# Kernel optimization log

Hardware: AMD Instinct MI355X
Metric: run time of the kernel (lower is better)

Reference implementation:

```python
import jax, jax.numpy as jnp
import numpy as np

N_NODES = 50000
N_EDGES = 800000
D_IN = 96
D_OUT = 96


def setup_inputs() -> dict:
    key = jax.random.key(0)
    k1, k2, k3, k4, k5, k6 = jax.random.split(key, 6)
    x = jax.random.normal(k1, (N_NODES, D_IN), dtype=jnp.float32)
    edge_index = jax.random.randint(k2, (2, N_EDGES), 0, N_NODES, dtype=jnp.int32)
    W_lin = jax.random.normal(k3, (D_OUT, D_IN), dtype=jnp.float32) * 0.1
    b_lin = jax.random.normal(k4, (D_OUT,), dtype=jnp.float32) * 0.1
    W_root = jax.random.normal(k5, (D_OUT, D_IN), dtype=jnp.float32) * 0.1
    b_root = jax.random.normal(k6, (D_OUT,), dtype=jnp.float32) * 0.1
    return {"x": x, "edge_index": edge_index, "W_lin": W_lin, "b_lin": b_lin,
            "W_root": W_root, "b_root": b_root}


def reference(x, edge_index, W_lin, b_lin, W_root, b_root):
    # GCNConv with separate root weight: out = relu(scatter_add(norm * lin(x_src), dst) + root(x))
    src, dst = edge_index[0], edge_index[1]
    n = x.shape[0]
    # symmetric degree normalization (in-degree based, clamped to avoid div0)
    deg = jax.ops.segment_sum(jnp.ones(src.shape[0], dtype=x.dtype), dst, num_segments=n)
    dinv = jax.lax.rsqrt(jnp.maximum(deg, 1.0))
    norm = dinv[src] * dinv[dst]                      # [E]
    h = x @ W_lin.T + b_lin                           # [N, D_OUT] neighbor transform
    msgs = h[src] * norm[:, None]                     # [E, D_OUT] gathered + scaled
    agg = jax.ops.segment_sum(msgs, dst, num_segments=n)  # scatter-add
    out = agg + x @ W_root.T + b_root                 # root/self contribution
    return jax.nn.relu(out)
```

## Files before the change

kernel.cpp:

```cpp
#include <hip/hip_runtime.h>

#define D 96
#define BSH 5
#define SCAP 1088
#define SBSH 8
#define NSBMAX 224
#define SBCAP 4608
#define CH 2048

typedef __attribute__((ext_vector_type(8))) short bf16x8;
typedef __attribute__((ext_vector_type(4))) float f32x4;

__device__ __forceinline__ unsigned bf16_rne(float f) {
    unsigned u = __float_as_uint(f);
    return (u + 0x7fffu + ((u >> 16) & 1u)) >> 16;
}
__device__ __forceinline__ float blo(unsigned u) { return __uint_as_float(u << 16); }
__device__ __forceinline__ float bhi(unsigned u) { return __uint_as_float(u & 0xffff0000u); }

__global__ __launch_bounds__(512) void bin_kernel(
    const int* __restrict__ ei, int* __restrict__ scur, unsigned* __restrict__ sp,
    const float* __restrict__ Wlin, const float* __restrict__ Wroot,
    unsigned* __restrict__ wfrag, int E, int NSB)
{
    __shared__ int hist[NSBMAX];
    __shared__ int lstart[NSBMAX];
    __shared__ int gbase[NSBMAX];
    __shared__ unsigned stage[CH];
    int t = threadIdx.x;
    int gt = blockIdx.x * 512 + t;
    int e0 = blockIdx.x * CH;
    int ne = min(CH, E - e0);
    for (int i = t; i < NSB; i += 512) hist[i] = 0;
    if (gt < 9216) {
        int f = gt >> 8, r = gt & 255;
        int l = r >> 2, jp = r & 3;
        int ct = f / 6, st = f % 6;
        int nn = ct * 16 + (l & 15);
        int k  = st * 32 + (l >> 4) * 8 + jp * 2;
        const float* W = (k < D) ? Wlin : Wroot;
        int kk = (k < D) ? k : k - D;
        float v0 = W[nn * D + kk], v1 = W[nn * D + kk + 1];
        wfrag[gt] = bf16_rne(v0) | (bf16_rne(v1) << 16);
    }
    __syncthreads();
    unsigned pk[4]; int bk[4];
    int base = e0 + t * 4;
    if (base + 3 < E) {
        int4 a = *(const int4*)(ei + base);
        int4 b = *(const int4*)(ei + E + base);
        pk[0] = (unsigned)a.x | ((unsigned)b.x << 16); bk[0] = b.x >> SBSH;
        pk[1] = (unsigned)a.y | ((unsigned)b.y << 16); bk[1] = b.y >> SBSH;
        pk[2] = (unsigned)a.z | ((unsigned)b.z << 16); bk[2] = b.z >> SBSH;
        pk[3] = (unsigned)a.w | ((unsigned)b.w << 16); bk[3] = b.w >> SBSH;
    } else {
        #pragma unroll
        for (int u = 0; u < 4; ++u) {
            int e = base + u;
            if (e < E) { pk[u] = (unsigned)ei[e] | ((unsigned)ei[E + e] << 16); bk[u] = ei[E + e] >> SBSH; }
            else bk[u] = -1;
        }
    }
    #pragma unroll
    for (int u = 0; u < 4; ++u)
        if (bk[u] >= 0) atomicAdd(&hist[bk[u]], 1);
    __syncthreads();
    if (t < 64) {
        int carry = 0;
        for (int c0 = 0; c0 < NSB; c0 += 64) {
            int i = c0 + t;
            int v = (i < NSB) ? hist[i] : 0;
            int incl = v;
            #pragma unroll
            for (int d = 1; d < 64; d <<= 1) {
                int uu = __shfl_up(incl, d, 64);
                if (t >= d) incl += uu;
            }
            if (i < NSB) lstart[i] = carry + incl - v;
            carry += __shfl(incl, 63, 64);
        }
    }
    __syncthreads();
    for (int i = t; i < NSB; i += 512) {
        int c = hist[i];
        if (c > 0) gbase[i] = atomicAdd(&scur[i], c);
        hist[i] = lstart[i];
    }
    __syncthreads();
    #pragma unroll
    for (int u = 0; u < 4; ++u) {
        if (bk[u] >= 0) {
            int p = atomicAdd(&hist[bk[u]], 1);
            stage[p] = pk[u];
        }
    }
    __syncthreads();
    for (int i = t; i < ne; i += 512) {
        unsigned w = stage[i];
        int sb = (int)(w >> (16 + SBSH));
        int slot = gbase[sb] + (i - lstart[sb]);
        if (slot < SBCAP) sp[(size_t)sb * SBCAP + slot] = w;
    }
}

__global__ __launch_bounds__(256) void xspack_kernel(
    const float* __restrict__ x, unsigned* __restrict__ xs, int n)
{
    int gt = blockIdx.x * 256 + threadIdx.x;
    int gsz = gridDim.x * 256;
    int ntask = (n + 1) * 24;
    for (int i = gt; i < ntask; i += gsz) {
        int row = i / 24, q = i - row * 24;
        uint2 o;
        if (row < n) {
            float4 v = ((const float4*)x)[(size_t)row * 24 + q];
            o.x = bf16_rne(v.x) | (bf16_rne(v.y) << 16);
            o.y = bf16_rne(v.z) | (bf16_rne(v.w) << 16);
        } else { o.x = 0u; o.y = 0u; }
        *(uint2*)(xs + (size_t)row * 48 + q * 2) = o;
    }
}

__global__ __launch_bounds__(512) void dinv_kernel(
    const int* __restrict__ scur, const unsigned* __restrict__ sp,
    float* __restrict__ dinv, int n)
{
    __shared__ int hist[256];
    int t = threadIdx.x;
    if (t < 256) hist[t] = 0;
    __syncthreads();
    int ne = min(scur[blockIdx.x], SBCAP);
    const unsigned* spb = sp + (size_t)blockIdx.x * SBCAP;
    for (int i0 = t * 4; i0 < ne; i0 += 2048) {
        if (i0 + 3 < ne) {
            uint4 w = *(const uint4*)(spb + i0);
            atomicAdd(&hist[(w.x >> 16) & 255], 1);
            atomicAdd(&hist[(w.y >> 16) & 255], 1);
            atomicAdd(&hist[(w.z >> 16) & 255], 1);
            atomicAdd(&hist[(w.w >> 16) & 255], 1);
        } else {
            for (int i = i0; i < ne; ++i) atomicAdd(&hist[(spb[i] >> 16) & 255], 1);
        }
    }
    __syncthreads();
    if (t < 256) {
        int node = (blockIdx.x << SBSH) + t;
        if (node < n) {
            int d = hist[t];
            dinv[node] = rsqrtf((float)(d > 1 ? d : 1));
        }
    }
    if (blockIdx.x == 0 && t == 256) dinv[n] = 0.f;
}

__global__ __launch_bounds__(256, 8) void bgather_gemm_kernel(
    const int* __restrict__ scur, const unsigned* __restrict__ sp,
    const float* __restrict__ dinv, const unsigned* __restrict__ xs,
    const unsigned* __restrict__ wfrag, const float* __restrict__ blin,
    const float* __restrict__ broot, float* __restrict__ out, int n)
{
    __shared__ uint2 sd[SCAP];
    __shared__ int hist[32];
    __shared__ int seg[33];
    __shared__ int cur[32];
    __shared__ int pq;
    __shared__ unsigned yt[32][52];
    __shared__ float sv32[32];
    int t = threadIdx.x;
    int nwg = gridDim.x;
    int qq = nwg >> 3, rr = nwg & 7;
    int xcd = blockIdx.x & 7, ix = blockIdx.x >> 3;
    int bid = (xcd < rr ? xcd * (qq + 1) : rr * (qq + 1) + (xcd - rr) * qq) + ix;
    int node0 = bid << BSH;
    int sb = bid >> 3;
    int lb = bid & 7;
    int ne = min(scur[sb], SBCAP);
    const unsigned* spb = sp + (size_t)sb * SBCAP;
    const unsigned ZR = (unsigned)n;
    if (t < 32) hist[t] = 0;
    if (t < 8) sd[t] = make_uint2(ZR, 0u);
    __syncthreads();
    for (int i0 = t * 4; i0 < ne; i0 += 1024) {
        if (i0 + 3 < ne) {
            uint4 w4 = *(const uint4*)(spb + i0);
            if (((w4.x >> (16 + BSH)) & 7) == (unsigned)lb) atomicAdd(&hist[(w4.x >> 16) & 31], 1);
            if (((w4.y >> (16 + BSH)) & 7) == (unsigned)lb) atomicAdd(&hist[(w4.y >> 16) & 31], 1);
            if (((w4.z >> (16 + BSH)) & 7) == (unsigned)lb) atomicAdd(&hist[(w4.z >> 16) & 31], 1);
            if (((w4.w >> (16 + BSH)) & 7) == (unsigned)lb) atomicAdd(&hist[(w4.w >> 16) & 31], 1);
        } else {
            for (int i = i0; i < ne; ++i) {
                unsigned w = spb[i];
                if (((w >> (16 + BSH)) & 7) == (unsigned)lb) atomicAdd(&hist[(w >> 16) & 31], 1);
            }
        }
    }
    __syncthreads();
    if (t == 0) {
        int run = 8;
        #pragma unroll
        for (int i = 0; i < 32; ++i) {
            seg[i] = run;
            run += (hist[i] + 7) & ~7;
            if (run > SCAP) run = SCAP;
        }
        seg[32] = run;
        pq = 0;
    }
    __syncthreads();
    if (t < 32) cur[t] = seg[t];
    __syncthreads();
    for (int i0 = t * 4; i0 < ne; i0 += 1024) {
        if (i0 + 3 < ne) {
            uint4 w4 = *(const uint4*)(spb + i0);
            if (((w4.x >> (16 + BSH)) & 7) == (unsigned)lb) { int p = atomicAdd(&cur[(w4.x >> 16) & 31], 1); if (p < SCAP) sd[p].x = w4.x & 0xffffu; }
            if (((w4.y >> (16 + BSH)) & 7) == (unsigned)lb) { int p = atomicAdd(&cur[(w4.y >> 16) & 31], 1); if (p < SCAP) sd[p].x = w4.y & 0xffffu; }
            if (((w4.z >> (16 + BSH)) & 7) == (unsigned)lb) { int p = atomicAdd(&cur[(w4.z >> 16) & 31], 1); if (p < SCAP) sd[p].x = w4.z & 0xffffu; }
            if (((w4.w >> (16 + BSH)) & 7) == (unsigned)lb) { int p = atomicAdd(&cur[(w4.w >> 16) & 31], 1); if (p < SCAP) sd[p].x = w4.w & 0xffffu; }
        } else {
            for (int i = i0; i < ne; ++i) {
                unsigned w = spb[i];
                if (((w >> (16 + BSH)) & 7) == (unsigned)lb) { int p = atomicAdd(&cur[(w >> 16) & 31], 1); if (p < SCAP) sd[p].x = w & 0xffffu; }
            }
        }
    }
    __syncthreads();
    if (t < 32) {
        int e = seg[t + 1];
        int s = seg[t] + hist[t]; if (s > e) s = e;
        for (int p2 = s; p2 < e; ++p2) sd[p2] = make_uint2(ZR, 0u);
    }
    __syncthreads();
    int tot = seg[32];
    for (int i = t; i < tot; i += 256) sd[i].y = __float_as_uint(dinv[sd[i].x]);
    __syncthreads();

    int l = t & 63;
    int g = l / 12;
    int m = l - g * 12;
    unsigned loff = (unsigned)(m << 4);
    const char* xb = (const char*)xs;

    for (;;) {
        int p;
        if (l == 0) p = atomicAdd(&pq, 1);
        p = __builtin_amdgcn_readfirstlane(p);
        if (p >= 16) break;
        int ndA = p * 2, ndB = ndA + 1;
        int jsA = seg[ndA], itA = (seg[ndA + 1] - jsA) >> 3;
        int jsB = seg[ndB], itB = (seg[ndB + 1] - jsB) >> 3;
        int iters = itA > itB ? itA : itB;
        float aA0=0.f,aA1=0.f,aA2=0.f,aA3=0.f,aA4=0.f,aA5=0.f,aA6=0.f,aA7=0.f;
        float aB0=0.f,aB1=0.f,aB2=0.f,aB3=0.f,aB4=0.f,aB5=0.f,aB6=0.f,aB7=0.f;
        float sn = 0.f;
        for (int it = 0; it < iters; ++it) {
            int baseA = (it < itA) ? (jsA + it * 8) : 0;
            int baseB = (it < itB) ? (jsB + it * 8) : 0;
            if (l < 48) {
                uint2 qA0 = sd[baseA + g], qA1 = sd[baseA + 4 + g];
                uint2 qB0 = sd[baseB + g], qB1 = sd[baseB + 4 + g];
                uint4 vA0 = *(const uint4*)(xb + qA0.x * 192u + loff);
                uint4 vA1 = *(const uint4*)(xb + qA1.x * 192u + loff);
                uint4 vB0 = *(const uint4*)(xb + qB0.x * 192u + loff);
                uint4 vB1 = *(const uint4*)(xb + qB1.x * 192u + loff);
                float dA0 = __uint_as_float(qA0.y), dA1 = __uint_as_float(qA1.y);
                float dB0 = __uint_as_float(qB0.y), dB1 = __uint_as_float(qB1.y);
                aA0 += dA0 * blo(vA0.x); aA1 += dA0 * bhi(vA0.x); aA2 += dA0 * blo(vA0.y); aA3 += dA0 * bhi(vA0.y);
                aA4 += dA0 * blo(vA0.z); aA5 += dA0 * bhi(vA0.z); aA6 += dA0 * blo(vA0.w); aA7 += dA0 * bhi(vA0.w);
                aA0 += dA1 * blo(vA1.x); aA1 += dA1 * bhi(vA1.x); aA2 += dA1 * blo(vA1.y); aA3 += dA1 * bhi(vA1.y);
                aA4 += dA1 * blo(vA1.z); aA5 += dA1 * bhi(vA1.z); aA6 += dA1 * blo(vA1.w); aA7 += dA1 * bhi(vA1.w);
                aB0 += dB0 * blo(vB0.x); aB1 += dB0 * bhi(vB0.x); aB2 += dB0 * blo(vB0.y); aB3 += dB0 * bhi(vB0.y);
                aB4 += dB0 * blo(vB0.z); aB5 += dB0 * bhi(vB0.z); aB6 += dB0 * blo(vB0.w); aB7 += dB0 * bhi(vB0.w);
                aB0 += dB1 * blo(vB1.x); aB1 += dB1 * bhi(vB1.x); aB2 += dB1 * blo(vB1.y); aB3 += dB1 * bhi(vB1.y);
                aB4 += dB1 * blo(vB1.z); aB5 += dB1 * bhi(vB1.z); aB6 += dB1 * blo(vB1.w); aB7 += dB1 * bhi(vB1.w);
            } else {
                int bs = (l < 56) ? baseA : baseB;
                sn += __uint_as_float(sd[bs + (l & 7)].y);
            }
        }
        float stA = 0.f, stB = 0.f;
        #pragma unroll
        for (int u = 0; u < 8; ++u) {
            stA += __shfl(sn, 48 + u, 64);
            stB += __shfl(sn, 56 + u, 64);
        }
        int l24 = (l + 24) & 63, l12 = (l + 12) & 63;
        aA0 += __shfl(aA0, l24, 64); aA1 += __shfl(aA1, l24, 64); aA2 += __shfl(aA2, l24, 64); aA3 += __shfl(aA3, l24, 64);
        aA4 += __shfl(aA4, l24, 64); aA5 += __shfl(aA5, l24, 64); aA6 += __shfl(aA6, l24, 64); aA7 += __shfl(aA7, l24, 64);
        aB0 += __shfl(aB0, l24, 64); aB1 += __shfl(aB1, l24, 64); aB2 += __shfl(aB2, l24, 64); aB3 += __shfl(aB3, l24, 64);
        aB4 += __shfl(aB4, l24, 64); aB5 += __shfl(aB5, l24, 64); aB6 += __shfl(aB6, l24, 64); aB7 += __shfl(aB7, l24, 64);
        aA0 += __shfl(aA0, l12, 64); aA1 += __shfl(aA1, l12, 64); aA2 += __shfl(aA2, l12, 64); aA3 += __shfl(aA3, l12, 64);
        aA4 += __shfl(aA4, l12, 64); aA5 += __shfl(aA5, l12, 64); aA6 += __shfl(aA6, l12, 64); aA7 += __shfl(aA7, l12, 64);
        aB0 += __shfl(aB0, l12, 64); aB1 += __shfl(aB1, l12, 64); aB2 += __shfl(aB2, l12, 64); aB3 += __shfl(aB3, l12, 64);
        aB4 += __shfl(aB4, l12, 64); aB5 += __shfl(aB5, l12, 64); aB6 += __shfl(aB6, l12, 64); aB7 += __shfl(aB7, l12, 64);
        int nodeA = node0 + ndA, nodeB = node0 + ndB;
        float dnA = (nodeA < n) ? dinv[nodeA] : 0.f;
        float dnB = (nodeB < n) ? dinv[nodeB] : 0.f;
        if (l < 12) {
            uint4 oA, oB;
            oA.x = bf16_rne(dnA * aA0) | (bf16_rne(dnA * aA1) << 16);
            oA.y = bf16_rne(dnA * aA2) | (bf16_rne(dnA * aA3) << 16);
            oA.z = bf16_rne(dnA * aA4) | (bf16_rne(dnA * aA5) << 16);
            oA.w = bf16_rne(dnA * aA6) | (bf16_rne(dnA * aA7) << 16);
            oB.x = bf16_rne(dnB * aB0) | (bf16_rne(dnB * aB1) << 16);
            oB.y = bf16_rne(dnB * aB2) | (bf16_rne(dnB * aB3) << 16);
            oB.z = bf16_rne(dnB * aB4) | (bf16_rne(dnB * aB5) << 16);
            oB.w = bf16_rne(dnB * aB6) | (bf16_rne(dnB * aB7) << 16);
            *(uint4*)&yt[ndA][4 * m] = oA;
            *(uint4*)&yt[ndB][4 * m] = oB;
        } else if (l == 48) {
            sv32[ndA] = dnA * stA;
            sv32[ndB] = dnB * stB;
        }
    }
    __syncthreads();

    int wv = t >> 6;
    int lane15 = l & 15, quad = l >> 4;
    for (int j = wv; j < 12; j += 4) {
        int rg = j / 6, ct = j % 6;
        int r0 = node0 + rg * 16;
        f32x4 accY = (f32x4){0.f, 0.f, 0.f, 0.f};
        f32x4 accX = (f32x4){0.f, 0.f, 0.f, 0.f};
        #pragma unroll
        for (int st_ = 0; st_ < 3; ++st_) {
            bf16x8 a = *(const bf16x8*)(&yt[rg * 16 + lane15][st_ * 16 + quad * 4]);
            bf16x8 b = *(const bf16x8*)(wfrag + ((ct * 6 + st_) * 64 + l) * 4);
            accY = __builtin_amdgcn_mfma_f32_16x16x32_bf16(a, b, accY, 0, 0, 0);
        }
        int ar = r0 + lane15;
        #pragma unroll
        for (int sm = 0; sm < 3; ++sm) {
            bf16x8 a = (bf16x8){0, 0, 0, 0, 0, 0, 0, 0};
            if (ar < n) a = *(const bf16x8*)(xs + (size_t)ar * 48 + sm * 16 + quad * 4);
            bf16x8 b = *(const bf16x8*)(wfrag + ((ct * 6 + 3 + sm) * 64 + l) * 4);
            accX = __builtin_amdgcn_mfma_f32_16x16x32_bf16(a, b, accX, 0, 0, 0);
        }
        int col = ct * 16 + lane15;
        float blc = blin[col], brc = broot[col];
        #pragma unroll
        for (int reg = 0; reg < 4; ++reg) {
            int r = r0 + quad * 4 + reg;
            if (r < n) {
                float sv = sv32[rg * 16 + quad * 4 + reg];
                float v = accY[reg] + accX[reg] + sv * blc + brc;
                out[(size_t)r * D + col] = fmaxf(v, 0.f);
            }
        }
    }
}

extern "C" void kernel_launch(void* const* d_in, const int* in_sizes, int n_in,
                              void* d_out, int out_size, void* d_ws, size_t ws_size,
                              hipStream_t stream) {
    const float* x     = (const float*)d_in[0];
    const int*   ei    = (const int*)d_in[1];
    const float* Wlin  = (const float*)d_in[2];
    const float* blin  = (const float*)d_in[3];
    const float* Wroot = (const float*)d_in[4];
    const float* broot = (const float*)d_in[5];
    float* out = (float*)d_out;

    const int n = in_sizes[0] / D;
    const int E = in_sizes[1] / 2;
    const int NB = (n + 31) >> BSH;
    const int NSB = (n + 255) >> SBSH;

    int*      scur  = (int*)d_ws;
    float*    dinv  = (float*)(scur + 256);
    unsigned* sp    = (unsigned*)(dinv + n + 4);
    unsigned* wfrag = sp + (size_t)NSB * SBCAP;
    unsigned* xs    = wfrag + 9216;

    hipMemsetAsync(scur, 0, 256 * sizeof(int), stream);

    bin_kernel<<<(E + CH - 1) / CH, 512, 0, stream>>>(ei, scur, sp, Wlin, Wroot,
                                                      wfrag, E, NSB);
    xspack_kernel<<<1024, 256, 0, stream>>>(x, xs, n);
    dinv_kernel<<<NSB, 512, 0, stream>>>(scur, sp, dinv, n);
    bgather_gemm_kernel<<<NB, 256, 0, stream>>>(scur, sp, dinv, xs, wfrag,
                                                blin, broot, out, n);
}
```

Baseline: 141.2 us.

## Replace atomic bucket binning with deterministic histogram-scan-scatter passes

The single binning kernel, which claimed global slots through atomics on per-bucket counters, is split into three passes. A histogram kernel writes per-block bucket counts, a scan kernel computes per-bucket block offsets, and a scatter kernel places edges at those offsets. The x-to-bf16 packing is folded into the histogram kernel and the memset is dropped. This removes global atomics and gives deterministic edge ordering within each bucket, but adds a kernel launch and reads the edge index twice.

New measurement: 143.0 us. About the same (+1.3%).

```diff
diff --git a/kernel.cpp b/kernel.cpp
--- a/kernel.cpp
+++ b/kernel.cpp
@@ -18,19 +18,16 @@
 __device__ __forceinline__ float blo(unsigned u) { return __uint_as_float(u << 16); }
 __device__ __forceinline__ float bhi(unsigned u) { return __uint_as_float(u & 0xffff0000u); }
 
-__global__ __launch_bounds__(512) void bin_kernel(
-    const int* __restrict__ ei, int* __restrict__ scur, unsigned* __restrict__ sp,
+__global__ __launch_bounds__(512) void hist_kernel(
+    const int* __restrict__ ei, int* __restrict__ ghist,
     const float* __restrict__ Wlin, const float* __restrict__ Wroot,
-    unsigned* __restrict__ wfrag, int E, int NSB)
+    unsigned* __restrict__ wfrag, const float* __restrict__ x,
+    unsigned* __restrict__ xs, int E, int NSB, int NBLK, int n)
 {
     __shared__ int hist[NSBMAX];
-    __shared__ int lstart[NSBMAX];
-    __shared__ int gbase[NSBMAX];
-    __shared__ unsigned stage[CH];
     int t = threadIdx.x;
     int gt = blockIdx.x * 512 + t;
     int e0 = blockIdx.x * CH;
-    int ne = min(CH, E - e0);
     for (int i = t; i < NSB; i += 512) hist[i] = 0;
     if (gt < 9216) {
         int f = gt >> 8, r = gt & 255;
@@ -43,6 +40,70 @@
         float v0 = W[nn * D + kk], v1 = W[nn * D + kk + 1];
         wfrag[gt] = bf16_rne(v0) | (bf16_rne(v1) << 16);
     }
+    __syncthreads();
+    int base = e0 + t * 4;
+    if (base + 3 < E) {
+        int4 b = *(const int4*)(ei + E + base);
+        atomicAdd(&hist[b.x >> SBSH], 1);
+        atomicAdd(&hist[b.y >> SBSH], 1);
+        atomicAdd(&hist[b.z >> SBSH], 1);
+        atomicAdd(&hist[b.w >> SBSH], 1);
+    } else {
+        for (int u = 0; u < 4; ++u) {
+            int e = base + u;
+            if (e < E) atomicAdd(&hist[ei[E + e] >> SBSH], 1);
+        }
+    }
+    __syncthreads();
+    for (int i = t; i < NSB; i += 512) ghist[(size_t)i * NBLK + blockIdx.x] = hist[i];
+    int gsz = gridDim.x * 512;
+    int ntask = (n + 1) * 24;
+    for (int i = gt; i < ntask; i += gsz) {
+        int row = i / 24, q = i - row * 24;
+        uint2 o;
+        if (row < n) {
+            float4 v = ((const float4*)x)[(size_t)row * 24 + q];
+            o.x = bf16_rne(v.x) | (bf16_rne(v.y) << 16);
+            o.y = bf16_rne(v.z) | (bf16_rne(v.w) << 16);
+        } else { o.x = 0u; o.y = 0u; }
+        *(uint2*)(xs + (size_t)row * 48 + q * 2) = o;
+    }
+}
+
+__global__ __launch_bounds__(64) void scan_kernel(
+    int* __restrict__ ghist, int* __restrict__ scur, int NBLK)
+{
+    int t = threadIdx.x;
+    int* row = ghist + (size_t)blockIdx.x * NBLK;
+    int carry = 0;
+    for (int c0 = 0; c0 < NBLK; c0 += 64) {
+        int i = c0 + t;
+        int v = (i < NBLK) ? row[i] : 0;
+        int incl = v;
+        #pragma unroll
+        for (int d = 1; d < 64; d <<= 1) {
+            int uu = __shfl_up(incl, d, 64);
+            if (t >= d) incl += uu;
+        }
+        if (i < NBLK) row[i] = carry + incl - v;
+        carry += __shfl(incl, 63, 64);
+    }
+    if (t == 0) scur[blockIdx.x] = carry;
+}
+
+__global__ __launch_bounds__(512) void scatter_kernel(
+    const int* __restrict__ ei, const int* __restrict__ ghist,
+    unsigned* __restrict__ sp, int E, int NSB, int NBLK)
+{
+    __shared__ int hist[NSBMAX];
+    __shared__ int lstart[NSBMAX];
+    __shared__ int gb[NSBMAX];
+    __shared__ unsigned stage[CH];
+    int t = threadIdx.x;
+    int blk = blockIdx.x;
+    int e0 = blk * CH;
+    int ne = min(CH, E - e0);
+    for (int i = t; i < NSB; i += 512) hist[i] = 0;
     __syncthreads();
     unsigned pk[4]; int bk[4];
     int base = e0 + t * 4;
@@ -82,8 +143,7 @@
     }
     __syncthreads();
     for (int i = t; i < NSB; i += 512) {
-        int c = hist[i];
-        if (c > 0) gbase[i] = atomicAdd(&scur[i], c);
+        gb[i] = ghist[(size_t)i * NBLK + blk];
         hist[i] = lstart[i];
     }
     __syncthreads();
@@ -98,26 +158,8 @@
     for (int i = t; i < ne; i += 512) {
         unsigned w = stage[i];
         int sb = (int)(w >> (16 + SBSH));
-        int slot = gbase[sb] + (i - lstart[sb]);
+        int slot = gb[sb] + (i - lstart[sb]);
         if (slot < SBCAP) sp[(size_t)sb * SBCAP + slot] = w;
-    }
-}
-
-__global__ __launch_bounds__(256) void xspack_kernel(
-    const float* __restrict__ x, unsigned* __restrict__ xs, int n)
-{
-    int gt = blockIdx.x * 256 + threadIdx.x;
-    int gsz = gridDim.x * 256;
-    int ntask = (n + 1) * 24;
-    for (int i = gt; i < ntask; i += gsz) {
-        int row = i / 24, q = i - row * 24;
-        uint2 o;
-        if (row < n) {
-            float4 v = ((const float4*)x)[(size_t)row * 24 + q];
-            o.x = bf16_rne(v.x) | (bf16_rne(v.y) << 16);
-            o.y = bf16_rne(v.z) | (bf16_rne(v.w) << 16);
-        } else { o.x = 0u; o.y = 0u; }
-        *(uint2*)(xs + (size_t)row * 48 + q * 2) = o;
     }
 }
 
@@ -364,18 +406,19 @@
     const int E = in_sizes[1] / 2;
     const int NB = (n + 31) >> BSH;
     const int NSB = (n + 255) >> SBSH;
+    const int NBLK = (E + CH - 1) / CH;
 
     int*      scur  = (int*)d_ws;
     float*    dinv  = (float*)(scur + 256);
     unsigned* sp    = (unsigned*)(dinv + n + 4);
     unsigned* wfrag = sp + (size_t)NSB * SBCAP;
     unsigned* xs    = wfrag + 9216;
-
-    hipMemsetAsync(scur, 0, 256 * sizeof(int), stream);
-
-    bin_kernel<<<(E + CH - 1) / CH, 512, 0, stream>>>(ei, scur, sp, Wlin, Wroot,
-                                                      wfrag, E, NSB);
-    xspack_kernel<<<1024, 256, 0, stream>>>(x, xs, n);
+    int*      ghist = (int*)(xs + (size_t)(n + 1) * 48);
+
+    hist_kernel<<<NBLK, 512, 0, stream>>>(ei, ghist, Wlin, Wroot, wfrag,
+                                          x, xs, E, NSB, NBLK, n);
+    scan_kernel<<<NSB, 64, 0, stream>>>(ghist, scur, NBLK);
+    scatter_kernel<<<NBLK, 512, 0, stream>>>(ei, ghist, sp, E, NSB, NBLK);
     dinv_kernel<<<NSB, 512, 0, stream>>>(scur, sp, dinv, n);
     bgather_gemm_kernel<<<NB, 256, 0, stream>>>(scur, sp, dinv, xs, wfrag,
                                                 blin, broot, out, n);
```

## Fuse binning, packing, degree and gather-GEMM into one cooperative kernel

Applied to the files above, without the earlier changes.

Merges the four separate launches (edge binning, x bf16 packing, degree/dinv, gather+MFMA GEMM) into one persistent kernel with grid-wide syncs between phases. The aim is to remove launch gaps and kernel-boundary drains. Binning now runs at 256 threads with 8 edges per thread, and all phases share one raw shared-memory buffer. If cooperative launch fails, it falls back to three launches selected by mask. Risks: grid sync cost, NB=1563 blocks must all be co-resident (7 per CU), and occupancy drops from 8 to 7 blocks per CU.

Result: slower. 498.7 us (+253.3%).

```diff
diff --git a/kernel.cpp b/kernel.cpp
--- a/kernel.cpp
+++ b/kernel.cpp
@@ -1,4 +1,7 @@
 #include <hip/hip_runtime.h>
+#include <hip/hip_cooperative_groups.h>
+
+namespace cg = cooperative_groups;
 
 #define D 96
 #define BSH 5
@@ -7,6 +10,7 @@
 #define NSBMAX 224
 #define SBCAP 4608
 #define CH 2048
+#define SMBYTES 15888
 
 typedef __attribute__((ext_vector_type(8))) short bf16x8;
 typedef __attribute__((ext_vector_type(4))) float f32x4;
@@ -18,332 +22,322 @@
 __device__ __forceinline__ float blo(unsigned u) { return __uint_as_float(u << 16); }
 __device__ __forceinline__ float bhi(unsigned u) { return __uint_as_float(u & 0xffff0000u); }
 
-__global__ __launch_bounds__(512) void bin_kernel(
+__global__ __launch_bounds__(256, 7) void fused_kernel(
     const int* __restrict__ ei, int* __restrict__ scur, unsigned* __restrict__ sp,
     const float* __restrict__ Wlin, const float* __restrict__ Wroot,
-    unsigned* __restrict__ wfrag, int E, int NSB)
+    unsigned* __restrict__ wfrag, const float* __restrict__ x,
+    unsigned* __restrict__ xs, float* __restrict__ dinv, int* __restrict__ deg,
+    const float* __restrict__ blin, const float* __restrict__ broot,
+    float* __restrict__ out, int E, int NSB, int NBLK, int n, int mask)
 {
-    __shared__ int hist[NSBMAX];
-    __shared__ int lstart[NSBMAX];
-    __shared__ int gbase[NSBMAX];
-    __shared__ unsigned stage[CH];
+    __shared__ __attribute__((aligned(16))) char smraw[SMBYTES];
     int t = threadIdx.x;
-    int gt = blockIdx.x * 512 + t;
-    int e0 = blockIdx.x * CH;
-    int ne = min(CH, E - e0);
-    for (int i = t; i < NSB; i += 512) hist[i] = 0;
-    if (gt < 9216) {
-        int f = gt >> 8, r = gt & 255;
-        int l = r >> 2, jp = r & 3;
-        int ct = f / 6, st = f % 6;
-        int nn = ct * 16 + (l & 15);
-        int k  = st * 32 + (l >> 4) * 8 + jp * 2;
-        const float* W = (k < D) ? Wlin : Wroot;
-        int kk = (k < D) ? k : k - D;
-        float v0 = W[nn * D + kk], v1 = W[nn * D + kk + 1];
-        wfrag[gt] = bf16_rne(v0) | (bf16_rne(v1) << 16);
+    int blk = blockIdx.x;
+
+    if (mask & 1) {
+        int gt = blk * 256 + t;
+        if (gt < 9216) {
+            int f = gt >> 8, r = gt & 255;
+            int l = r >> 2, jp = r & 3;
+            int ct = f / 6, st = f % 6;
+            int nn = ct * 16 + (l & 15);
+            int k  = st * 32 + (l >> 4) * 8 + jp * 2;
+            const float* W = (k < D) ? Wlin : Wroot;
+            int kk = (k < D) ? k : k - D;
+            float v0 = W[nn * D + kk], v1 = W[nn * D + kk + 1];
+            wfrag[gt] = bf16_rne(v0) | (bf16_rne(v1) << 16);
+        }
+        if (blk < NBLK) {
+            int* histA   = (int*)smraw;
+            int* lstartA = histA + NSBMAX;
+            int* gbaseA  = lstartA + NSBMAX;
+            unsigned* stageA = (unsigned*)(gbaseA + NSBMAX);
+            int e0 = blk * CH;
+            int ne = min(CH, E - e0);
+            for (int i = t; i < NSB; i += 256) histA[i] = 0;
+            __syncthreads();
+            unsigned pk[8]; int bk[8];
+            int base = e0 + t * 8;
+            #pragma unroll
+            for (int q = 0; q < 2; ++q) {
+                int b4 = base + q * 4;
+                if (b4 + 3 < E) {
+                    int4 a = *(const int4*)(ei + b4);
+                    int4 b = *(const int4*)(ei + E + b4);
+                    pk[q*4+0] = (unsigned)a.x | ((unsigned)b.x << 16); bk[q*4+0] = b.x >> SBSH;
+                    pk[q*4+1] = (unsigned)a.y | ((unsigned)b.y << 16); bk[q*4+1] = b.y >> SBSH;
+                    pk[q*4+2] = (unsigned)a.z | ((unsigned)b.z << 16); bk[q*4+2] = b.z >> SBSH;
+                    pk[q*4+3] = (unsigned)a.w | ((unsigned)b.w << 16); bk[q*4+3] = b.w >> SBSH;
+                } else {
+                    #pragma unroll
+                    for (int u = 0; u < 4; ++u) {
+                        int e = b4 + u;
+                        if (e < E) { pk[q*4+u] = (unsigned)ei[e] | ((unsigned)ei[E + e] << 16); bk[q*4+u] = ei[E + e] >> SBSH; }
+                        else bk[q*4+u] = -1;
+                    }
+                }
+            }
+            #pragma unroll
+            for (int u = 0; u < 8; ++u)
+                if (bk[u] >= 0) atomicAdd(&histA[bk[u]], 1);
+            __syncthreads();
+            if (t < 64) {
+                int carry = 0;
+                for (int c0 = 0; c0 < NSB; c0 += 64) {
+                    int i = c0 + t;
+                    int v = (i < NSB) ? histA[i] : 0;
+                    int incl = v;
+                    #pragma unroll
+                    for (int d = 1; d < 64; d <<= 1) {
+                        int uu = __shfl_up(incl, d, 64);
+                        if (t >= d) incl += uu;
+                    }
+                    if (i < NSB) lstartA[i] = carry + incl - v;
+                    carry += __shfl(incl, 63, 64);
+                }
+            }
+            __syncthreads();
+            for (int i = t; i < NSB; i += 256) {
+                int c = histA[i];
+                if (c > 0) gbaseA[i] = atomicAdd(&scur[i], c);
+                histA[i] = lstartA[i];
+            }
+            __syncthreads();
+            #pragma unroll
+            for (int u = 0; u < 8; ++u) {
+                if (bk[u] >= 0) {
+                    int p = atomicAdd(&histA[bk[u]], 1);
+                    stageA[p] = pk[u];
+                }
+            }
+            __syncthreads();
+            for (int i = t; i < ne; i += 256) {
+                unsigned w = stageA[i];
+                int sb = (int)(w >> (16 + SBSH));
+                int slot = gbaseA[sb] + (i - lstartA[sb]);
+                if (slot < SBCAP) sp[(size_t)sb * SBCAP + slot] = w;
+            }
+        }
+        int gsz = gridDim.x * 256;
+        int ntask = (n + 1) * 24;
+        for (int i = blk * 256 + t; i < ntask; i += gsz) {
+            int row = i / 24, q = i - row * 24;
+            uint2 o;
+            if (row < n) {
+                float4 v = ((const float4*)x)[(size_t)row * 24 + q];
+                o.x = bf16_rne(v.x) | (bf16_rne(v.y) << 16);
+                o.y = bf16_rne(v.z) | (bf16_rne(v.w) << 16);
+            } else { o.x = 0u; o.y = 0u; }
+            *(uint2*)(xs + (size_t)row * 48 + q * 2) = o;
+        }
     }
-    __syncthreads();
-    unsigned pk[4]; int bk[4];
-    int base = e0 + t * 4;
-    if (base + 3 < E) {
-        int4 a = *(const int4*)(ei + base);
-        int4 b = *(const int4*)(ei + E + base);
-        pk[0] = (unsigned)a.x | ((unsigned)b.x << 16); bk[0] = b.x >> SBSH;
-        pk[1] = (unsigned)a.y | ((unsigned)b.y << 16); bk[1] = b.y >> SBSH;
-        pk[2] = (unsigned)a.z | ((unsigned)b.z << 16); bk[2] = b.z >> SBSH;
-        pk[3] = (unsigned)a.w | ((unsigned)b.w << 16); bk[3] = b.w >> SBSH;
-    } else {
-        #pragma unroll
-        for (int u = 0; u < 4; ++u) {
-            int e = base + u;
-            if (e < E) { pk[u] = (unsigned)ei[e] | ((unsigned)ei[E + e] << 16); bk[u] = ei[E + e] >> SBSH; }
-            else bk[u] = -1;
+    if (mask == 7) cg::this_grid().sync();
+
+    if (mask & 2) {
+        if (blk < NSB) {
+            int* histB = (int*)smraw;
+            histB[t] = 0;
+            __syncthreads();
+            int ne = min(scur[blk], SBCAP);
+            const unsigned* spb = sp + (size_t)blk * SBCAP;
+            for (int i0 = t * 4; i0 < ne; i0 += 1024) {
+                if (i0 + 3 < ne) {
+                    uint4 w = *(const uint4*)(spb + i0);
+                    atomicAdd(&histB[(w.x >> 16) & 255], 1);
+                    atomicAdd(&histB[(w.y >> 16) & 255], 1);
+                    atomicAdd(&histB[(w.z >> 16) & 255], 1);
+                    atomicAdd(&histB[(w.w >> 16) & 255], 1);
+                } else {
+                    for (int i = i0; i < ne; ++i) atomicAdd(&histB[(spb[i] >> 16) & 255], 1);
+                }
+            }
+            __syncthreads();
+            int node = (blk << SBSH) + t;
+            if (node < n) {
+                int d = histB[t];
+                deg[node] = d;
+                dinv[node] = rsqrtf((float)(d > 1 ? d : 1));
+            }
+            if (blk == 0 && t == 0) { dinv[n] = 0.f; deg[n] = 0; }
         }
     }
-    #pragma unroll
-    for (int u = 0; u < 4; ++u)
-        if (bk[u] >= 0) atomicAdd(&hist[bk[u]], 1);
-    __syncthreads();
-    if (t < 64) {
-        int carry = 0;
-        for (int c0 = 0; c0 < NSB; c0 += 64) {
-            int i = c0 + t;
-            int v = (i < NSB) ? hist[i] : 0;
-            int incl = v;
-            #pragma unroll
-            for (int d = 1; d < 64; d <<= 1) {
-                int uu = __shfl_up(incl, d, 64);
-                if (t >= d) incl += uu;
-            }
-            if (i < NSB) lstart[i] = carry + incl - v;
-            carry += __shfl(incl, 63, 64);
-        }
-    }
-    __syncthreads();
-    for (int i = t; i < NSB; i += 512) {
-        int c = hist[i];
-        if (c > 0) gbase[i] = atomicAdd(&scur[i], c);
-        hist[i] = lstart[i];
-    }
-    __syncthreads();
-    #pragma unroll
-    for (int u = 0; u < 4; ++u) {
-        if (bk[u] >= 0) {
-            int p = atomicAdd(&hist[bk[u]], 1);
-            stage[p] = pk[u];
-        }
-    }
-    __syncthreads();
-    for (int i = t; i < ne; i += 512) {
-        unsigned w = stage[i];
-        int sb = (int)(w >> (16 + SBSH));
-        int slot = gbase[sb] + (i - lstart[sb]);
-        if (slot < SBCAP) sp[(size_t)sb * SBCAP + slot] = w;
-    }
-}
-
-__global__ __launch_bounds__(256) void xspack_kernel(
-    const float* __restrict__ x, unsigned* __restrict__ xs, int n)
-{
-    int gt = blockIdx.x * 256 + threadIdx.x;
-    int gsz = gridDim.x * 256;
-    int ntask = (n + 1) * 24;
-    for (int i = gt; i < ntask; i += gsz) {
-        int row = i / 24, q = i - row * 24;
-        uint2 o;
-        if (row < n) {
-            float4 v = ((const float4*)x)[(size_t)row * 24 + q];
-            o.x = bf16_rne(v.x) | (bf16_rne(v.y) << 16);
-            o.y = bf16_rne(v.z) | (bf16_rne(v.w) << 16);
-        } else { o.x = 0u; o.y = 0u; }
-        *(uint2*)(xs + (size_t)row * 48 + q * 2) = o;
-    }
-}
-
-__global__ __launch_bounds__(512) void dinv_kernel(
-    const int* __restrict__ scur, const unsigned* __restrict__ sp,
-    float* __restrict__ dinv, int n)
-{
-    __shared__ int hist[256];
-    int t = threadIdx.x;
-    if (t < 256) hist[t] = 0;
-    __syncthreads();
-    int ne = min(scur[blockIdx.x], SBCAP);
-    const unsigned* spb = sp + (size_t)blockIdx.x * SBCAP;
-    for (int i0 = t * 4; i0 < ne; i0 += 2048) {
-        if (i0 + 3 < ne) {
-            uint4 w = *(const uint4*)(spb + i0);
-            atomicAdd(&hist[(w.x >> 16) & 255], 1);
-            atomicAdd(&hist[(w.y >> 16) & 255], 1);
-            atomicAdd(&hist[(w.z >> 16) & 255], 1);
-            atomicAdd(&hist[(w.w >> 16) & 255], 1);
-        } else {
-            for (int i = i0; i < ne; ++i) atomicAdd(&hist[(spb[i] >> 16) & 255], 1);
-        }
-    }
-    __syncthreads();
-    if (t < 256) {
-        int node = (blockIdx.x << SBSH) + t;
-        if (node < n) {
-            int d = hist[t];
-            dinv[node] = rsqrtf((float)(d > 1 ? d : 1));
-        }
-    }
-    if (blockIdx.x == 0 && t == 256) dinv[n] = 0.f;
-}
-
-__global__ __launch_bounds__(256, 8) void bgather_gemm_kernel(
-    const int* __restrict__ scur, const unsigned* __restrict__ sp,
-    const float* __restrict__ dinv, const unsigned* __restrict__ xs,
-    const unsigned* __restrict__ wfrag, const float* __restrict__ blin,
-    const float* __restrict__ broot, float* __restrict__ out, int n)
-{
-    __shared__ uint2 sd[SCAP];
-    __shared__ int hist[32];
-    __shared__ int seg[33];
-    __shared__ int cur[32];
-    __shared__ int pq;
-    __shared__ unsigned yt[32][52];
-    __shared__ float sv32[32];
-    int t = threadIdx.x;
-    int nwg = gridDim.x;
-    int qq = nwg >> 3, rr = nwg & 7;
-    int xcd = blockIdx.x & 7, ix = blockIdx.x >> 3;
-    int bid = (xcd < rr ? xcd * (qq + 1) : rr * (qq + 1) + (xcd - rr) * qq) + ix;
-    int node0 = bid << BSH;
-    int sb = bid >> 3;
-    int lb = bid & 7;
-    int ne = min(scur[sb], SBCAP);
-    const unsigned* spb = sp + (size_t)sb * SBCAP;
-    const unsigned ZR = (unsigned)n;
-    if (t < 32) hist[t] = 0;
-    if (t < 8) sd[t] = make_uint2(ZR, 0u);
-    __syncthreads();
-    for (int i0 = t * 4; i0 < ne; i0 += 1024) {
-        if (i0 + 3 < ne) {
-            uint4 w4 = *(const uint4*)(spb + i0);
-            if (((w4.x >> (16 + BSH)) & 7) == (unsigned)lb) atomicAdd(&hist[(w4.x >> 16) & 31], 1);
-            if (((w4.y >> (16 + BSH)) & 7) == (unsigned)lb) atomicAdd(&hist[(w4.y >> 16) & 31], 1);
-            if (((w4.z >> (16 + BSH)) & 7) == (unsigned)lb) atomicAdd(&hist[(w4.z >> 16) & 31], 1);
-            if (((w4.w >> (16 + BSH)) & 7) == (unsigned)lb) atomicAdd(&hist[(w4.w >> 16) & 31], 1);
-        } else {
-            for (int i = i0; i < ne; ++i) {
-                unsigned w = spb[i];
-                if (((w >> (16 + BSH)) & 7) == (unsigned)lb) atomicAdd(&hist[(w >> 16) & 31], 1);
-            }
-        }
-    }
-    __syncthreads();
-    if (t == 0) {
-        int run = 8;
-        #pragma unroll
-        for (int i = 0; i < 32; ++i) {
-            seg[i] = run;
-            run += (hist[i] + 7) & ~7;
-            if (run > SCAP) run = SCAP;
-        }
-        seg[32] = run;
-        pq = 0;
-    }
-    __syncthreads();
-    if (t < 32) cur[t] = seg[t];
-    __syncthreads();
-    for (int i0 = t * 4; i0 < ne; i0 += 1024) {
-        if (i0 + 3 < ne) {
-            uint4 w4 = *(const uint4*)(spb + i0);
-            if (((w4.x >> (16 + BSH)) & 7) == (unsigned)lb) { int p = atomicAdd(&cur[(w4.x >> 16) & 31], 1); if (p < SCAP) sd[p].x = w4.x & 0xffffu; }
-            if (((w4.y >> (16 + BSH)) & 7) == (unsigned)lb) { int p = atomicAdd(&cur[(w4.y >> 16) & 31], 1); if (p < SCAP) sd[p].x = w4.y & 0xffffu; }
-            if (((w4.z >> (16 + BSH)) & 7) == (unsigned)lb) { int p = atomicAdd(&cur[(w4.z >> 16) & 31], 1); if (p < SCAP) sd[p].x = w4.z & 0xffffu; }
-            if (((w4.w >> (16 + BSH)) & 7) == (unsigned)lb) { int p = atomicAdd(&cur[(w4.w >> 16) & 31], 1); if (p < SCAP) sd[p].x = w4.w & 0xffffu; }
-        } else {
-            for (int i = i0; i < ne; ++i) {
-                unsigned w = spb[i];
-                if (((w >> (16 + BSH)) & 7) == (unsigned)lb) { int p = atomicAdd(&cur[(w >> 16) & 31], 1); if (p < SCAP) sd[p].x = w & 0xffffu; }
-            }
-        }
-    }
-    __syncthreads();
-    if (t < 32) {
-        int e = seg[t + 1];
-        int s = seg[t] + hist[t]; if (s > e) s = e;
-        for (int p2 = s; p2 < e; ++p2) sd[p2] = make_uint2(ZR, 0u);
-    }
-    __syncthreads();
-    int tot = seg[32];
-    for (int i = t; i < tot; i += 256) sd[i].y = __float_as_uint(dinv[sd[i].x]);
-    __syncthreads();
-
-    int l = t & 63;
-    int g = l / 12;
-    int m = l - g * 12;
-    unsigned loff = (unsigned)(m << 4);
-    const char* xb = (const char*)xs;
-
-    for (;;) {
-        int p;
-        if (l == 0) p = atomicAdd(&pq, 1);
-        p = __builtin_amdgcn_readfirstlane(p);
-        if (p >= 16) break;
-        int ndA = p * 2, ndB = ndA + 1;
-        int jsA = seg[ndA], itA = (seg[ndA + 1] - jsA) >> 3;
-        int jsB = seg[ndB], itB = (seg[ndB + 1] - jsB) >> 3;
-        int iters = itA > itB ? itA : itB;
-        float aA0=0.f,aA1=0.f,aA2=0.f,aA3=0.f,aA4=0.f,aA5=0.f,aA6=0.f,aA7=0.f;
-        float aB0=0.f,aB1=0.f,aB2=0.f,aB3=0.f,aB4=0.f,aB5=0.f,aB6=0.f,aB7=0.f;
-        float sn = 0.f;
-        for (int it = 0; it < iters; ++it) {
-            int baseA = (it < itA) ? (jsA + it * 8) : 0;
-            int baseB = (it < itB) ? (jsB + it * 8) : 0;
-            if (l < 48) {
-                uint2 qA0 = sd[baseA + g], qA1 = sd[baseA + 4 + g];
-                uint2 qB0 = sd[baseB + g], qB1 = sd[baseB + 4 + g];
-                uint4 vA0 = *(const uint4*)(xb + qA0.x * 192u + loff);
-                uint4 vA1 = *(const uint4*)(xb + qA1.x * 192u + loff);
-                uint4 vB0 = *(const uint4*)(xb + qB0.x * 192u + loff);
-                uint4 vB1 = *(const uint4*)(xb + qB1.x * 192u + loff);
-                float dA0 = __uint_as_float(qA0.y), dA1 = __uint_as_float(qA1.y);
-                float dB0 = __uint_as_float(qB0.y), dB1 = __uint_as_float(qB1.y);
-                aA0 += dA0 * blo(vA0.x); aA1 += dA0 * bhi(vA0.x); aA2 += dA0 * blo(vA0.y); aA3 += dA0 * bhi(vA0.y);
-                aA4 += dA0 * blo(vA0.z); aA5 += dA0 * bhi(vA0.z); aA6 += dA0 * blo(vA0.w); aA7 += dA0 * bhi(vA0.w);
-                aA0 += dA1 * blo(vA1.x); aA1 += dA1 * bhi(vA1.x); aA2 += dA1 * blo(vA1.y); aA3 += dA1 * bhi(vA1.y);
-                aA4 += dA1 * blo(vA1.z); aA5 += dA1 * bhi(vA1.z); aA6 += dA1 * blo(vA1.w); aA7 += dA1 * bhi(vA1.w);
-                aB0 += dB0 * blo(vB0.x); aB1 += dB0 * bhi(vB0.x); aB2 += dB0 * blo(vB0.y); aB3 += dB0 * bhi(vB0.y);
-                aB4 += dB0 * blo(vB0.z); aB5 += dB0 * bhi(vB0.z); aB6 += dB0 * blo(vB0.w); aB7 += dB0 * bhi(vB0.w);
-                aB0 += dB1 * blo(vB1.x); aB1 += dB1 * bhi(vB1.x); aB2 += dB1 * blo(vB1.y); aB3 += dB1 * bhi(vB1.y);
-                aB4 += dB1 * blo(vB1.z); aB5 += dB1 * bhi(vB1.z); aB6 += dB1 * blo(vB1.w); aB7 += dB1 * bhi(vB1.w);
+    if (mask == 7) cg::this_grid().sync();
+
+    if (mask & 4) {
+        uint2* sd   = (uint2*)smraw;
+        int* histC  = (int*)(smraw + 8704);
+        int* seg    = histC + 32;
+        int* cur    = seg + 33;
+        int* pqp    = cur + 32;
+        float* sv32 = (float*)(pqp + 1);
+        unsigned* ytb = (unsigned*)(smraw + 9232);
+
+        int nwg = gridDim.x;
+        int qq = nwg >> 3, rr = nwg & 7;
+        int xcd = blk & 7, ix = blk >> 3;
+        int bid = (xcd < rr ? xcd * (qq + 1) : rr * (qq + 1) + (xcd - rr) * qq) + ix;
+        int node0 = bid << BSH;
+        int sb = bid >> 3;
+        int lb = bid & 7;
+        int ne = min(scur[sb], SBCAP);
+        const unsigned* spb = sp + (size_t)sb * SBCAP;
+        const unsigned ZR = (unsigned)n;
+        if (t < 32) {
+            int node = node0 + t;
+            histC[t] = (node < n) ? deg[node] : 0;
+        }
+        if (t >= 32 && t < 40) sd[t - 32] = make_uint2(ZR, 0u);
+        __syncthreads();
+        if (t == 0) {
+            int run = 8;
+            #pragma unroll
+            for (int i = 0; i < 32; ++i) {
+                seg[i] = run;
+                run += (histC[i] + 7) & ~7;
+                if (run > SCAP) run = SCAP;
+            }
+            seg[32] = run;
+            *pqp = 0;
+        }
+        __syncthreads();
+        if (t < 32) cur[t] = seg[t];
+        __syncthreads();
+        for (int i0 = t * 4; i0 < ne; i0 += 1024) {
+            if (i0 + 3 < ne) {
+                uint4 w4 = *(const uint4*)(spb + i0);
+                if (((w4.x >> (16 + BSH)) & 7) == (unsigned)lb) { int p = atomicAdd(&cur[(w4.x >> 16) & 31], 1); if (p < SCAP) sd[p].x = w4.x & 0xffffu; }
+                if (((w4.y >> (16 + BSH)) & 7) == (unsigned)lb) { int p = atomicAdd(&cur[(w4.y >> 16) & 31], 1); if (p < SCAP) sd[p].x = w4.y & 0xffffu; }
+                if (((w4.z >> (16 + BSH)) & 7) == (unsigned)lb) { int p = atomicAdd(&cur[(w4.z >> 16) & 31], 1); if (p < SCAP) sd[p].x = w4.z & 0xffffu; }
+                if (((w4.w >> (16 + BSH)) & 7) == (unsigned)lb) { int p = atomicAdd(&cur[(w4.w >> 16) & 31], 1); if (p < SCAP) sd[p].x = w4.w & 0xffffu; }
             } else {
-                int bs = (l < 56) ? baseA : baseB;
-                sn += __uint_as_float(sd[bs + (l & 7)].y);
-            }
-        }
-        float stA = 0.f, stB = 0.f;
-        #pragma unroll
-        for (int u = 0; u < 8; ++u) {
-            stA += __shfl(sn, 48 + u, 64);
-            stB += __shfl(sn, 56 + u, 64);
-        }
-        int l24 = (l + 24) & 63, l12 = (l + 12) & 63;
-        aA0 += __shfl(aA0, l24, 64); aA1 += __shfl(aA1, l24, 64); aA2 += __shfl(aA2, l24, 64); aA3 += __shfl(aA3, l24, 64);
-        aA4 += __shfl(aA4, l24, 64); aA5 += __shfl(aA5, l24, 64); aA6 += __shfl(aA6, l24, 64); aA7 += __shfl(aA7, l24, 64);
-        aB0 += __shfl(aB0, l24, 64); aB1 += __shfl(aB1, l24, 64); aB2 += __shfl(aB2, l24, 64); aB3 += __shfl(aB3, l24, 64);
-        aB4 += __shfl(aB4, l24, 64); aB5 += __shfl(aB5, l24, 64); aB6 += __shfl(aB6, l24, 64); aB7 += __shfl(aB7, l24, 64);
-        aA0 += __shfl(aA0, l12, 64); aA1 += __shfl(aA1, l12, 64); aA2 += __shfl(aA2, l12, 64); aA3 += __shfl(aA3, l12, 64);
-        aA4 += __shfl(aA4, l12, 64); aA5 += __shfl(aA5, l12, 64); aA6 += __shfl(aA6, l12, 64); aA7 += __shfl(aA7, l12, 64);
-        aB0 += __shfl(aB0, l12, 64); aB1 += __shfl(aB1, l12, 64); aB2 += __shfl(aB2, l12, 64); aB3 += __shfl(aB3, l12, 64);
-        aB4 += __shfl(aB4, l12, 64); aB5 += __shfl(aB5, l12, 64); aB6 += __shfl(aB6, l12, 64); aB7 += __shfl(aB7, l12, 64);
-        int nodeA = node0 + ndA, nodeB = node0 + ndB;
-        float dnA = (nodeA < n) ? dinv[nodeA] : 0.f;
-        float dnB = (nodeB < n) ? dinv[nodeB] : 0.f;
-        if (l < 12) {
-            uint4 oA, oB;
-            oA.x = bf16_rne(dnA * aA0) | (bf16_rne(dnA * aA1) << 16);
-            oA.y = bf16_rne(dnA * aA2) | (bf16_rne(dnA * aA3) << 16);
-            oA.z = bf16_rne(dnA * aA4) | (bf16_rne(dnA * aA5) << 16);
-            oA.w = bf16_rne(dnA * aA6) | (bf16_rne(dnA * aA7) << 16);
-            oB.x = bf16_rne(dnB * aB0) | (bf16_rne(dnB * aB1) << 16);
-            oB.y = bf16_rne(dnB * aB2) | (bf16_rne(dnB * aB3) << 16);
-            oB.z = bf16_rne(dnB * aB4) | (bf16_rne(dnB * aB5) << 16);
-            oB.w = bf16_rne(dnB * aB6) | (bf16_rne(dnB * aB7) << 16);
-            *(uint4*)&yt[ndA][4 * m] = oA;
-            *(uint4*)&yt[ndB][4 * m] = oB;
-        } else if (l == 48) {
-            sv32[ndA] = dnA * stA;
-            sv32[ndB] = dnB * stB;
-        }
-    }
-    __syncthreads();
-
-    int wv = t >> 6;
-    int lane15 = l & 15, quad = l >> 4;
-    for (int j = wv; j < 12; j += 4) {
-        int rg = j / 6, ct = j % 6;
-        int r0 = node0 + rg * 16;
-        f32x4 accY = (f32x4){0.f, 0.f, 0.f, 0.f};
-        f32x4 accX = (f32x4){0.f, 0.f, 0.f, 0.f};
-        #pragma unroll
-        for (int st_ = 0; st_ < 3; ++st_) {
-            bf16x8 a = *(const bf16x8*)(&yt[rg * 16 + lane15][st_ * 16 + quad * 4]);
-            bf16x8 b = *(const bf16x8*)(wfrag + ((ct * 6 + st_) * 64 + l) * 4);
-            accY = __builtin_amdgcn_mfma_f32_16x16x32_bf16(a, b, accY, 0, 0, 0);
-        }
-        int ar = r0 + lane15;
-        #pragma unroll
-        for (int sm = 0; sm < 3; ++sm) {
-            bf16x8 a = (bf16x8){0, 0, 0, 0, 0, 0, 0, 0};
-            if (ar < n) a = *(const bf16x8*)(xs + (size_t)ar * 48 + sm * 16 + quad * 4);
-            bf16x8 b = *(const bf16x8*)(wfrag + ((ct * 6 + 3 + sm) * 64 + l) * 4);
-            accX = __builtin_amdgcn_mfma_f32_16x16x32_bf16(a, b, accX, 0, 0, 0);
-        }
-        int col = ct * 16 + lane15;
-        float blc = blin[col], brc = broot[col];
-        #pragma unroll
-        for (int reg = 0; reg < 4; ++reg) {
-            int r = r0 + quad * 4 + reg;
-            if (r < n) {
-                float sv = sv32[rg * 16 + quad * 4 + reg];
-                float v = accY[reg] + accX[reg] + sv * blc + brc;
-                out[(size_t)r * D + col] = fmaxf(v, 0.f);
+                for (int i = i0; i < ne; ++i) {
+                    unsigned w = spb[i];
+                    if (((w >> (16 + BSH)) & 7) == (unsigned)lb) { int p = atomicAdd(&cur[(w >> 16) & 31], 1); if (p < SCAP) sd[p].x = w & 0xffffu; }
+                }
+            }
+        }
+        __syncthreads();
+        if (t < 32) {
+            int e = seg[t + 1];
+            int s = seg[t] + histC[t]; if (s > e) s = e;
+            for (int p2 = s; p2 < e; ++p2) sd[p2] = make_uint2(ZR, 0u);
+        }
+        __syncthreads();
+        int tot = seg[32];
+        for (int i = t; i < tot; i += 256) sd[i].y = __float_as_uint(dinv[sd[i].x]);
+        __syncthreads();
+
+        int l = t & 63;
+        int g = l / 12;
+        int m = l - g * 12;
+        unsigned loff = (unsigned)(m << 4);
+        const char* xb = (const char*)xs;
+
+        for (;;) {
+            int p;
+            if (l == 0) p = atomicAdd(pqp, 1);
+            p = __builtin_amdgcn_readfirstlane(p);
+            if (p >= 16) break;
+            int ndA = p * 2, ndB = ndA + 1;
+            int jsA = seg[ndA], itA = (seg[ndA + 1] - jsA) >> 3;
+            int jsB = seg[ndB], itB = (seg[ndB + 1] - jsB) >> 3;
+            int iters = itA > itB ? itA : itB;
+            float aA0=0.f,aA1=0.f,aA2=0.f,aA3=0.f,aA4=0.f,aA5=0.f,aA6=0.f,aA7=0.f;
+            float aB0=0.f,aB1=0.f,aB2=0.f,aB3=0.f,aB4=0.f,aB5=0.f,aB6=0.f,aB7=0.f;
+            float sn = 0.f;
+            for (int it = 0; it < iters; ++it) {
+                int baseA = (it < itA) ? (jsA + it * 8) : 0;
+                int baseB = (it < itB) ? (jsB + it * 8) : 0;
+                if (l < 48) {
+                    uint2 qA0 = sd[baseA + g], qA1 = sd[baseA + 4 + g];
+                    uint2 qB0 = sd[baseB + g], qB1 = sd[baseB + 4 + g];
+                    uint4 vA0 = *(const uint4*)(xb + qA0.x * 192u + loff);
+                    uint4 vA1 = *(const uint4*)(xb + qA1.x * 192u + loff);
+                    uint4 vB0 = *(const uint4*)(xb + qB0.x * 192u + loff);
+                    uint4 vB1 = *(const uint4*)(xb + qB1.x * 192u + loff);
+                    float dA0 = __uint_as_float(qA0.y), dA1 = __uint_as_float(qA1.y);
+                    float dB0 = __uint_as_float(qB0.y), dB1 = __uint_as_float(qB1.y);
+                    aA0 += dA0 * blo(vA0.x); aA1 += dA0 * bhi(vA0.x); aA2 += dA0 * blo(vA0.y); aA3 += dA0 * bhi(vA0.y);
+                    aA4 += dA0 * blo(vA0.z); aA5 += dA0 * bhi(vA0.z); aA6 += dA0 * blo(vA0.w); aA7 += dA0 * bhi(vA0.w);
+                    aA0 += dA1 * blo(vA1.x); aA1 += dA1 * bhi(vA1.x); aA2 += dA1 * blo(vA1.y); aA3 += dA1 * bhi(vA1.y);
+                    aA4 += dA1 * blo(vA1.z); aA5 += dA1 * bhi(vA1.z); aA6 += dA1 * blo(vA1.w); aA7 += dA1 * bhi(vA1.w);
+                    aB0 += dB0 * blo(vB0.x); aB1 += dB0 * bhi(vB0.x); aB2 += dB0 * blo(vB0.y); aB3 += dB0 * bhi(vB0.y);
+                    aB4 += dB0 * blo(vB0.z); aB5 += dB0 * bhi(vB0.z); aB6 += dB0 * blo(vB0.w); aB7 += dB0 * bhi(vB0.w);
+                    aB0 += dB1 * blo(vB1.x); aB1 += dB1 * bhi(vB1.x); aB2 += dB1 * blo(vB1.y); aB3 += dB1 * bhi(vB1.y);
+                    aB4 += dB1 * blo(vB1.z); aB5 += dB1 * bhi(vB1.z); aB6 += dB1 * blo(vB1.w); aB7 += dB1 * bhi(vB1.w);
+                } else {
+                    int bs = (l < 56) ? baseA : baseB;
+                    sn += __uint_as_float(sd[bs + (l & 7)].y);
+                }
+            }
+            float stA = 0.f, stB = 0.f;
+            #pragma unroll
+            for (int u = 0; u < 8; ++u) {
+                stA += __shfl(sn, 48 + u, 64);
+                stB += __shfl(sn, 56 + u, 64);
+            }
+            int l24 = (l + 24) & 63, l12 = (l + 12) & 63;
+            aA0 += __shfl(aA0, l24, 64); aA1 += __shfl(aA1, l24, 64); aA2 += __shfl(aA2, l24, 64); aA3 += __shfl(aA3, l24, 64);
+            aA4 += __shfl(aA4, l24, 64); aA5 += __shfl(aA5, l24, 64); aA6 += __shfl(aA6, l24, 64); aA7 += __shfl(aA7, l24, 64);
+            aB0 += __shfl(aB0, l24, 64); aB1 += __shfl(aB1, l24, 64); aB2 += __shfl(aB2, l24, 64); aB3 += __shfl(aB3, l24, 64);
+            aB4 += __shfl(aB4, l24, 64); aB5 += __shfl(aB5, l24, 64); aB6 += __shfl(aB6, l24, 64); aB7 += __shfl(aB7, l24, 64);
+            aA0 += __shfl(aA0, l12, 64); aA1 += __shfl(aA1, l12, 64); aA2 += __shfl(aA2, l12, 64); aA3 += __shfl(aA3, l12, 64);
+            aA4 += __shfl(aA4, l12, 64); aA5 += __shfl(aA5, l12, 64); aA6 += __shfl(aA6, l12, 64); aA7 += __shfl(aA7, l12, 64);
+            aB0 += __shfl(aB0, l12, 64); aB1 += __shfl(aB1, l12, 64); aB2 += __shfl(aB2, l12, 64); aB3 += __shfl(aB3, l12, 64);
+            aB4 += __shfl(aB4, l12, 64); aB5 += __shfl(aB5, l12, 64); aB6 += __shfl(aB6, l12, 64); aB7 += __shfl(aB7, l12, 64);
+            int nodeA = node0 + ndA, nodeB = node0 + ndB;
+            float dnA = (nodeA < n) ? dinv[nodeA] : 0.f;
+            float dnB = (nodeB < n) ? dinv[nodeB] : 0.f;
+            if (l < 12) {
+                uint4 oA, oB;
+                oA.x = bf16_rne(dnA * aA0) | (bf16_rne(dnA * aA1) << 16);
+                oA.y = bf16_rne(dnA * aA2) | (bf16_rne(dnA * aA3) << 16);
+                oA.z = bf16_rne(dnA * aA4) | (bf16_rne(dnA * aA5) << 16);
+                oA.w = bf16_rne(dnA * aA6) | (bf16_rne(dnA * aA7) << 16);
+                oB.x = bf16_rne(dnB * aB0) | (bf16_rne(dnB * aB1) << 16);
+                oB.y = bf16_rne(dnB * aB2) | (bf16_rne(dnB * aB3) << 16);
+                oB.z = bf16_rne(dnB * aB4) | (bf16_rne(dnB * aB5) << 16);
+                oB.w = bf16_rne(dnB * aB6) | (bf16_rne(dnB * aB7) << 16);
+                *(uint4*)&ytb[ndA * 52 + 4 * m] = oA;
+                *(uint4*)&ytb[ndB * 52 + 4 * m] = oB;
+            } else if (l == 48) {
+                sv32[ndA] = dnA * stA;
+                sv32[ndB] = dnB * stB;
+            }
+        }
+        __syncthreads();
+
+        int wv = t >> 6;
+        int lane15 = l & 15, quad = l >> 4;
+        for (int j = wv; j < 12; j += 4) {
+            int rg = j / 6, ct = j % 6;
+            int r0 = node0 + rg * 16;
+            f32x4 accY = (f32x4){0.f, 0.f, 0.f, 0.f};
+            f32x4 accX = (f32x4){0.f, 0.f, 0.f, 0.f};
+            #pragma unroll
+            for (int st_ = 0; st_ < 3; ++st_) {
+                bf16x8 a = *(const bf16x8*)(&ytb[(rg * 16 + lane15) * 52 + st_ * 16 + quad * 4]);
+                bf16x8 b = *(const bf16x8*)(wfrag + ((ct * 6 + st_) * 64 + l) * 4);
+                accY = __builtin_amdgcn_mfma_f32_16x16x32_bf16(a, b, accY, 0, 0, 0);
+            }
+            int ar = r0 + lane15;
+            #pragma unroll
+            for (int sm = 0; sm < 3; ++sm) {
+                bf16x8 a = (bf16x8){0, 0, 0, 0, 0, 0, 0, 0};
+                if (ar < n) a = *(const bf16x8*)(xs + (size_t)ar * 48 + sm * 16 + quad * 4);
+                bf16x8 b = *(const bf16x8*)(wfrag + ((ct * 6 + 3 + sm) * 64 + l) * 4);
+                accX = __builtin_amdgcn_mfma_f32_16x16x32_bf16(a, b, accX, 0, 0, 0);
+            }
+            int col = ct * 16 + lane15;
+            float blc = blin[col], brc = broot[col];
+            #pragma unroll
+            for (int reg = 0; reg < 4; ++reg) {
+                int r = r0 + quad * 4 + reg;
+                if (r < n) {
+                    float sv = sv32[rg * 16 + quad * 4 + reg];
+                    float v = accY[reg] + accX[reg] + sv * blc + brc;
+                    out[(size_t)r * D + col] = fmaxf(v, 0.f);
+                }
             }
         }
     }
@@ -360,23 +354,35 @@
     const float* broot = (const float*)d_in[5];
     float* out = (float*)d_out;
 
-    const int n = in_sizes[0] / D;
-    const int E = in_sizes[1] / 2;
-    const int NB = (n + 31) >> BSH;
-    const int NSB = (n + 255) >> SBSH;
+    int n = in_sizes[0] / D;
+    int E = in_sizes[1] / 2;
+    int NB = (n + 31) >> BSH;
+    int NSB = (n + 255) >> SBSH;
+    int NBLK = (E + CH - 1) / CH;
 
     int*      scur  = (int*)d_ws;
     float*    dinv  = (float*)(scur + 256);
-    unsigned* sp    = (unsigned*)(dinv + n + 4);
+    int*      deg   = (int*)(dinv + n + 4);
+    unsigned* sp    = (unsigned*)(deg + n + 4);
     unsigned* wfrag = sp + (size_t)NSB * SBCAP;
     unsigned* xs    = wfrag + 9216;
 
     hipMemsetAsync(scur, 0, 256 * sizeof(int), stream);
 
-    bin_kernel<<<(E + CH - 1) / CH, 512, 0, stream>>>(ei, scur, sp, Wlin, Wroot,
-                                                      wfrag, E, NSB);
-    xspack_kernel<<<1024, 256, 0, stream>>>(x, xs, n);
-    dinv_kernel<<<NSB, 512, 0, stream>>>(scur, sp, dinv, n);
-    bgather_gemm_kernel<<<NB, 256, 0, stream>>>(scur, sp, dinv, xs, wfrag,
-                                                blin, broot, out, n);
+    int mask = 7;
+    void* kargs[] = { (void*)&ei, (void*)&scur, (void*)&sp, (void*)&Wlin, (void*)&Wroot,
+                      (void*)&wfrag, (void*)&x, (void*)&xs, (void*)&dinv, (void*)&deg,
+                      (void*)&blin, (void*)&broot, (void*)&out,
+                      (void*)&E, (void*)&NSB, (void*)&NBLK, (void*)&n, (void*)&mask };
+    hipError_t err = hipLaunchCooperativeKernel((void*)fused_kernel, dim3(NB), dim3(256),
+                                                kargs, 0, stream);
+    if (err != hipSuccess) {
+        (void)hipGetLastError();
+        fused_kernel<<<NB, 256, 0, stream>>>(ei, scur, sp, Wlin, Wroot, wfrag, x, xs,
+                                             dinv, deg, blin, broot, out, E, NSB, NBLK, n, 1);
+        fused_kernel<<<NB, 256, 0, stream>>>(ei, scur, sp, Wlin, Wroot, wfrag, x, xs,
+                                             dinv, deg, blin, broot, out, E, NSB, NBLK, n, 2);
+        fused_kernel<<<NB, 256, 0, stream>>>(ei, scur, sp, Wlin, Wroot, wfrag, x, xs,
+                                             dinv, deg, blin, broot, out, E, NSB, NBLK, n, 4);
+    }
 }
```
